# Kernel tuning notes

Hardware: AMD Instinct MI355X
Metric: run time of the kernel (lower is better)

Reference implementation:

```python
import jax, jax.numpy as jnp
import numpy as np

DIM = 128
KS = 7
HEADS = 4
HEAD_DIM = DIM // HEADS


def setup_inputs() -> dict:
    key = jax.random.key(0)
    ks = jax.random.split(key, 10)
    B, H, W, C = 4, 64, 64, DIM
    s = 0.02
    return {
        "x": jax.random.normal(ks[0], (B, H, W, C), jnp.float32),
        "qkv_w": jax.random.normal(ks[1], (C, 3 * C), jnp.float32) * s,
        "qkv_b": jnp.zeros((3 * C,), jnp.float32),
        "proj_w": jax.random.normal(ks[2], (C, C), jnp.float32) * s,
        "proj_b": jnp.zeros((C,), jnp.float32),
        "rpb": jax.random.normal(ks[3], (HEADS, 2 * KS - 1, 2 * KS - 1), jnp.float32) * s,
        "g1_w": jax.random.normal(ks[4], (C, C // 2), jnp.float32) * s,
        "g1_b": jnp.zeros((C // 2,), jnp.float32),
        "g2_w": jax.random.normal(ks[5], (C // 2, 1), jnp.float32) * s,
        "g2_b": jnp.zeros((1,), jnp.float32),
    }


def _neighborhood_attention(x, qkv_w, qkv_b, proj_w, proj_b, rpb):
    B, H, W, C = x.shape
    k = KS
    # qkv projection -> [B,H,W,3,heads,head_dim]
    qkv = (x @ qkv_w + qkv_b).reshape(B, H, W, 3, HEADS, HEAD_DIM)
    q = qkv[..., 0, :, :] * (HEAD_DIM ** -0.5)  # [B,H,W,h,d]
    kk = qkv[..., 1, :, :]
    v = qkv[..., 2, :, :]

    # Clamped sliding-window start indices (NATTEN semantics)
    sh = jnp.clip(jnp.arange(H) - k // 2, 0, H - k)  # [H]
    sw = jnp.clip(jnp.arange(W) - k // 2, 0, W - k)  # [W]
    idx_h = sh[:, None] + jnp.arange(k)[None, :]  # [H,k]
    idx_w = sw[:, None] + jnp.arange(k)[None, :]  # [W,k]

    # Gather neighborhood windows: [B,H,W,k,k,h,d]
    kwin = kk[:, idx_h[:, None, :, None], idx_w[None, :, None, :]]
    vwin = v[:, idx_h[:, None, :, None], idx_w[None, :, None, :]]

    # Relative position bias indices: (neighbor - query) + (k-1)
    bih = idx_h - jnp.arange(H)[:, None] + (k - 1)  # [H,k]
    biw = idx_w - jnp.arange(W)[:, None] + (k - 1)  # [W,k]
    # bias: [h,H,W,k,k] -> [H,W,h,k,k]
    bias = rpb[:, bih[:, None, :, None], biw[None, :, None, :]]
    bias = jnp.transpose(bias, (1, 2, 0, 3, 4))

    # scores: [B,H,W,h,k,k]
    scores = jnp.einsum('bxyhd,bxyklhd->bxyhkl', q, kwin) + bias[None]
    attn = jax.nn.softmax(scores.reshape(B, H, W, HEADS, k * k), axis=-1)
    attn = attn.reshape(B, H, W, HEADS, k, k)
    out = jnp.einsum('bxyhkl,bxyklhd->bxyhd', attn, vwin).reshape(B, H, W, C)
    return out @ proj_w + proj_b


def reference(x, qkv_w, qkv_b, proj_w, proj_b, rpb, g1_w, g1_b, g2_w, g2_b):
    attn_out = _neighborhood_attention(x, qkv_w, qkv_b, proj_w, proj_b, rpb)
    gate = jax.nn.sigmoid(jax.nn.relu(x @ g1_w + g1_b) @ g2_w + g2_b)  # [B,H,W,1]
    return attn_out * gate + x
```

## Files before the change

kernel.cpp:

```cpp
#include <hip/hip_runtime.h>
#include <hip/hip_bf16.h>
#include <math.h>

#define PIXELS 16384
#define C      128
#define KS     7
#define HEADS  4
#define HD     32
#define QSCALE 0.17677669529663687f

typedef __bf16 bf16x8 __attribute__((ext_vector_type(8)));
typedef float  f32x4  __attribute__((ext_vector_type(4)));

__device__ inline unsigned short f2bf(float f) {
    unsigned int u = __builtin_bit_cast(unsigned int, f);
    u += 0x7FFFu + ((u >> 16) & 1u);
    return (unsigned short)(u >> 16);
}
__device__ inline float bflo(unsigned int u) {
    return __builtin_bit_cast(float, u << 16);
}
__device__ inline float bfhi(unsigned int u) {
    return __builtin_bit_cast(float, u & 0xFFFF0000u);
}

__global__ __launch_bounds__(256) void prep_kernel(
    const float* __restrict__ x, const float* __restrict__ qkv_w,
    const float* __restrict__ g1_w, const float* __restrict__ qkv_b,
    const float* __restrict__ g1_b, const float* __restrict__ proj_w,
    unsigned short* __restrict__ xb, unsigned short* __restrict__ wT,
    unsigned short* __restrict__ pT, float* __restrict__ bias_ext)
{
    const int blk = blockIdx.x, tid = threadIdx.x;
    if (blk < 2048) {
        int base = blk * 1024 + tid * 4;
        float4 v = *(const float4*)(x + base);
        ushort4 o; o.x = f2bf(v.x); o.y = f2bf(v.y); o.z = f2bf(v.z); o.w = f2bf(v.w);
        *(ushort4*)(xb + base) = o;
    } else if (blk < 2104) {
        int n = (blk - 2048) * 8 + (tid >> 5);
        int kq = tid & 31;
        float f0, f1, f2, f3;
        if (n < 384) {
            f0 = qkv_w[(kq*4+0)*384 + n]; f1 = qkv_w[(kq*4+1)*384 + n];
            f2 = qkv_w[(kq*4+2)*384 + n]; f3 = qkv_w[(kq*4+3)*384 + n];
        } else {
            int nn = n - 384;
            f0 = g1_w[(kq*4+0)*64 + nn]; f1 = g1_w[(kq*4+1)*64 + nn];
            f2 = g1_w[(kq*4+2)*64 + nn]; f3 = g1_w[(kq*4+3)*64 + nn];
        }
        ushort4 o; o.x = f2bf(f0); o.y = f2bf(f1); o.z = f2bf(f2); o.w = f2bf(f3);
        *(ushort4*)(wT + n*128 + kq*4) = o;
    } else if (blk < 2120) {
        int n = (blk - 2104) * 8 + (tid >> 5);
        int kq = tid & 31;
        ushort4 o;
        o.x = f2bf(proj_w[(kq*4+0)*128 + n]);
        o.y = f2bf(proj_w[(kq*4+1)*128 + n]);
        o.z = f2bf(proj_w[(kq*4+2)*128 + n]);
        o.w = f2bf(proj_w[(kq*4+3)*128 + n]);
        *(ushort4*)(pT + n*128 + kq*4) = o;
    } else {
        for (int idx = tid; idx < 448; idx += 256)
            bias_ext[idx] = (idx < 384) ? qkv_b[idx] : g1_b[idx - 384];
    }
}

__global__ __launch_bounds__(256) void gemm_qkvh_fused(
    const unsigned short* __restrict__ xb, const unsigned short* __restrict__ wT,
    const float* __restrict__ bias_ext, const float* __restrict__ g2_w,
    const float* __restrict__ g2_b, unsigned short* __restrict__ qkvb,
    float* __restrict__ gate)
{
    __shared__ __align__(16) unsigned short As[64*128];
    __shared__ __align__(16) unsigned short Bs[64*128];
    const int nt = blockIdx.x;
    const int n0 = nt * 64;
    const int m0 = blockIdx.y * 64;
    const int tid = threadIdx.x;

#pragma unroll
    for (int it = 0; it < 4; it++) {
        int idx = tid + it*256, row = idx >> 4, c = idx & 15;
        uint4 v = *(const uint4*)(xb + (size_t)(m0+row)*128 + c*8);
        *(uint4*)(As + row*128 + ((c ^ (row&7)) << 3)) = v;
    }
#pragma unroll
    for (int it = 0; it < 4; it++) {
        int idx = tid + it*256, row = idx >> 4, c = idx & 15;
        uint4 v = *(const uint4*)(wT + (size_t)(n0+row)*128 + c*8);
        *(uint4*)(Bs + row*128 + ((c ^ (row&7)) << 3)) = v;
    }
    __syncthreads();

    const int wave = tid >> 6, lane = tid & 63;
    const int l15 = lane & 15, quad = lane >> 4;
    const int wm = (wave & 1) * 32, wn = (wave >> 1) * 32;

    f32x4 acc[2][2] = {};
#pragma unroll
    for (int ks = 0; ks < 4; ks++) {
        bf16x8 af[2], bq[2];
#pragma unroll
        for (int mt = 0; mt < 2; mt++) {
            int m = wm + mt*16 + l15;
            af[mt] = *(const bf16x8*)(As + m*128 + (((ks*4+quad) ^ (m&7)) << 3));
        }
#pragma unroll
        for (int ntl = 0; ntl < 2; ntl++) {
            int n = wn + ntl*16 + l15;
            bq[ntl] = *(const bf16x8*)(Bs + n*128 + (((ks*4+quad) ^ (n&7)) << 3));
        }
#pragma unroll
        for (int mt = 0; mt < 2; mt++)
#pragma unroll
            for (int ntl = 0; ntl < 2; ntl++)
                acc[mt][ntl] = __builtin_amdgcn_mfma_f32_16x16x32_bf16(
                    af[mt], bq[ntl], acc[mt][ntl], 0, 0, 0);
    }
    __syncthreads();

    if (nt < 6) {
        unsigned short* Cs = (unsigned short*)As;
#pragma unroll
        for (int ntl = 0; ntl < 2; ntl++) {
            int nl = wn + ntl*16 + l15;
            int ng = n0 + nl;
            float qs = (ng < 128) ? QSCALE : 1.0f;
            float bv = bias_ext[ng];
#pragma unroll
            for (int mt = 0; mt < 2; mt++)
#pragma unroll
                for (int r = 0; r < 4; r++) {
                    int ml = wm + mt*16 + quad*4 + r;
                    Cs[ml*64 + nl] = f2bf((acc[mt][ntl][r] + bv) * qs);
                }
        }
        __syncthreads();
        int row = tid >> 2, part = tid & 3;
        uint4 a = *(const uint4*)(Cs + row*64 + part*16);
        uint4 b = *(const uint4*)(Cs + row*64 + part*16 + 8);
        unsigned short* dst = qkvb + (size_t)(m0+row)*384 + n0 + part*16;
        *(uint4*)dst = a;
        *(uint4*)(dst + 8) = b;
    } else {
        float* gpart = (float*)Bs;
        float rs[2][4];
#pragma unroll
        for (int mt = 0; mt < 2; mt++)
#pragma unroll
            for (int r = 0; r < 4; r++) rs[mt][r] = 0.0f;
#pragma unroll
        for (int ntl = 0; ntl < 2; ntl++) {
            int nl = wn + ntl*16 + l15;
            float bv = bias_ext[384 + nl];
            float gw = g2_w[nl];
#pragma unroll
            for (int mt = 0; mt < 2; mt++)
#pragma unroll
                for (int r = 0; r < 4; r++) {
                    float h = acc[mt][ntl][r] + bv;
                    rs[mt][r] += fmaxf(h, 0.0f) * gw;
                }
        }
#pragma unroll
        for (int off = 1; off <= 8; off <<= 1)
#pragma unroll
            for (int mt = 0; mt < 2; mt++)
#pragma unroll
                for (int r = 0; r < 4; r++)
                    rs[mt][r] += __shfl_xor(rs[mt][r], off);
        if (l15 == 0) {
#pragma unroll
            for (int mt = 0; mt < 2; mt++)
#pragma unroll
                for (int r = 0; r < 4; r++)
                    gpart[(wave >> 1)*64 + wm + mt*16 + quad*4 + r] = rs[mt][r];
        }
        __syncthreads();
        if (tid < 64) {
            float g = gpart[tid] + gpart[64 + tid] + g2_b[0];
            gate[m0 + tid] = 1.0f / (1.0f + __expf(-g));
        }
    }
}

__global__ __launch_bounds__(256) void attn_kernel(
    const unsigned short* __restrict__ qkvb, const float* __restrict__ rpb,
    unsigned short* __restrict__ attnb)
{
    __shared__ __align__(16) unsigned short kvs[140 * 64];
    __shared__ float qf[32 * 32];
    __shared__ float rpb_lds[169];

    const int blk = blockIdx.x;
    const int h = blk & 3;
    const int tile = (blk >> 2) & 127;
    const int b = blk >> 9;
    const int tj0 = (tile & 15) * 4;
    const int ti0 = (tile >> 4) * 8;
    int wr0 = ti0 - 3; wr0 = wr0 < 0 ? 0 : (wr0 > 50 ? 50 : wr0);
    int wc0 = tj0 - 3; wc0 = wc0 < 0 ? 0 : (wc0 > 54 ? 54 : wc0);

    const int tid = threadIdx.x;

    if (tid < 169) rpb_lds[tid] = rpb[h * 169 + tid];

    if (tid < 128) {
        int pix = tid >> 2, jj = tid & 3;
        int pi = pix >> 2, pj = pix & 3;
        int gp = (b * 64 + ti0 + pi) * 64 + (tj0 + pj);
        uint4 u = *(const uint4*)(qkvb + (size_t)gp * 384 + h * 32 + jj * 8);
        float4 qa = { bflo(u.x), bfhi(u.x), bflo(u.y), bfhi(u.y) };
        float4 qb = { bflo(u.z), bfhi(u.z), bflo(u.w), bfhi(u.w) };
        *(float4*)(qf + pix*32 + jj*8)     = qa;
        *(float4*)(qf + pix*32 + jj*8 + 4) = qb;
    }
    for (int idx = tid; idx < 140 * 8; idx += 256) {
        int pos = idx >> 3, c = idx & 7;
        int rr = pos / 10, cc = pos - rr * 10;
        int gp = (b * 64 + wr0 + rr) * 64 + (wc0 + cc);
        int off = 128 + ((c >> 2) << 7) + h * 32 + ((c & 3) << 3);
        uint4 v = *(const uint4*)(qkvb + (size_t)gp * 384 + off);
        *(uint4*)(kvs + pos*64 + ((c ^ (pos & 7)) << 3)) = v;
    }
    __syncthreads();

    const int w = tid >> 6, lane = tid & 63;
    const int d4 = lane & 7, lg = lane >> 3;
    const int nr = (lane * 37) >> 8;
    const int nc = lane - nr * 7;

#pragma unroll 1
    for (int s = 0; s < 8; s++) {
        const int pix = w * 8 + s;
        const int pi = pix >> 2, pj = pix & 3;
        const int i = ti0 + pi, jx = tj0 + pj;
        int sh = i - 3; sh = sh < 0 ? 0 : (sh > 57 ? 57 : sh);
        int sw = jx - 3; sw = sw < 0 ? 0 : (sw > 57 ? 57 : sw);
        const int dr = sh - wr0, dc = sw - wc0;

        float e = 0.0f;
        if (lane < 49) {
            int pos = (dr + nr) * 10 + (dc + nc);
            int p7 = pos & 7;
            float acc = rpb_lds[(sh + nr - i + 6) * 13 + (sw + nc - jx + 6)];
            const float4* q4 = (const float4*)(qf + pix * 32);
#pragma unroll
            for (int c = 0; c < 4; c++) {
                uint4 k = *(const uint4*)(kvs + pos*64 + ((c ^ p7) << 3));
                float4 qa = q4[c*2], qb = q4[c*2+1];
                acc += qa.x*bflo(k.x) + qa.y*bfhi(k.x)
                     + qa.z*bflo(k.y) + qa.w*bfhi(k.y)
                     + qb.x*bflo(k.z) + qb.y*bfhi(k.z)
                     + qb.z*bflo(k.w) + qb.w*bfhi(k.w);
            }
            e = __expf(acc);
        }
        float sum = e;
#pragma unroll
        for (int off = 32; off >= 1; off >>= 1) sum += __shfl_xor(sum, off);
        const float a = e / sum;

        float4 acc4 = {0.f, 0.f, 0.f, 0.f};
#pragma unroll
        for (int t = 0; t < 7; t++) {
            int l = lg + 8 * t;
            float al = __shfl(a, l);
            int lr = (l * 37) >> 8, lc = l - lr * 7;
            int pos = (dr + lr) * 10 + (dc + lc);
            if (l >= 49) pos = 0;
            int p7 = pos & 7;
            uint2 v2 = *(const uint2*)(kvs + pos*64 +
                           (((4 + (d4 >> 1)) ^ p7) << 3) + ((d4 & 1) << 2));
            acc4.x += al * bflo(v2.x); acc4.y += al * bfhi(v2.x);
            acc4.z += al * bflo(v2.y); acc4.w += al * bfhi(v2.y);
        }
#pragma unroll
        for (int off = 8; off <= 32; off <<= 1) {
            acc4.x += __shfl_xor(acc4.x, off);
            acc4.y += __shfl_xor(acc4.y, off);
            acc4.z += __shfl_xor(acc4.z, off);
            acc4.w += __shfl_xor(acc4.w, off);
        }
        if (lg == 0) {
            int gp = (b * 64 + i) * 64 + jx;
            ushort4 o;
            o.x = f2bf(acc4.x); o.y = f2bf(acc4.y);
            o.z = f2bf(acc4.z); o.w = f2bf(acc4.w);
            *(ushort4*)(attnb + (size_t)gp * 128 + h * 32 + d4 * 4) = o;
        }
    }
}

__global__ __launch_bounds__(256) void gemm_proj_mfma(
    const unsigned short* __restrict__ ab, const unsigned short* __restrict__ pT,
    const float* __restrict__ proj_b, const float* __restrict__ gate,
    const float* __restrict__ x, float* __restrict__ out)
{
    __shared__ __align__(16) unsigned short As[64*128];
    __shared__ __align__(16) unsigned short Bs[64*128];
    const int n0 = blockIdx.x * 64;
    const int m0 = blockIdx.y * 64;
    const int tid = threadIdx.x;

#pragma unroll
    for (int it = 0; it < 4; it++) {
        int idx = tid + it*256, row = idx >> 4, c = idx & 15;
        uint4 v = *(const uint4*)(ab + (size_t)(m0+row)*128 + c*8);
        *(uint4*)(As + row*128 + ((c ^ (row&7)) << 3)) = v;
    }
#pragma unroll
    for (int it = 0; it < 4; it++) {
        int idx = tid + it*256, row = idx >> 4, c = idx & 15;
        uint4 v = *(const uint4*)(pT + (size_t)(n0+row)*128 + c*8);
        *(uint4*)(Bs + row*128 + ((c ^ (row&7)) << 3)) = v;
    }
    __syncthreads();

    const int wave = tid >> 6, lane = tid & 63;
    const int l15 = lane & 15, quad = lane >> 4;
    const int wm = (wave & 1) * 32, wn = (wave >> 1) * 32;

    f32x4 acc[2][2] = {};
#pragma unroll
    for (int ks = 0; ks < 4; ks++) {
        bf16x8 af[2], bq[2];
#pragma unroll
        for (int mt = 0; mt < 2; mt++) {
            int m = wm + mt*16 + l15;
            af[mt] = *(const bf16x8*)(As + m*128 + (((ks*4+quad) ^ (m&7)) << 3));
        }
#pragma unroll
        for (int ntl = 0; ntl < 2; ntl++) {
            int n = wn + ntl*16 + l15;
            bq[ntl] = *(const bf16x8*)(Bs + n*128 + (((ks*4+quad) ^ (n&7)) << 3));
        }
#pragma unroll
        for (int mt = 0; mt < 2; mt++)
#pragma unroll
            for (int ntl = 0; ntl < 2; ntl++)
                acc[mt][ntl] = __builtin_amdgcn_mfma_f32_16x16x32_bf16(
                    af[mt], bq[ntl], acc[mt][ntl], 0, 0, 0);
    }
    __syncthreads();

    float* Cs = (float*)As;
#pragma unroll
    for (int ntl = 0; ntl < 2; ntl++) {
        int nl = wn + ntl*16 + l15;
        float bv = proj_b[n0 + nl];
#pragma unroll
        for (int mt = 0; mt < 2; mt++)
#pragma unroll
            for (int r = 0; r < 4; r++) {
                int ml = wm + mt*16 + quad*4 + r;
                Cs[ml*64 + nl] = acc[mt][ntl][r] + bv;
            }
    }
    __syncthreads();
    int row = tid >> 2, part = tid & 3;
    float gv = gate[m0 + row];
    const float* xr = x + (size_t)(m0+row)*128 + n0 + part*16;
    float* orow = out + (size_t)(m0+row)*128 + n0 + part*16;
#pragma unroll
    for (int q = 0; q < 4; q++) {
        float4 cv = *(const float4*)(Cs + row*64 + part*16 + q*4);
        float4 xv = *(const float4*)(xr + q*4);
        float4 o;
        o.x = cv.x * gv + xv.x; o.y = cv.y * gv + xv.y;
        o.z = cv.z * gv + xv.z; o.w = cv.w * gv + xv.w;
        *(float4*)(orow + q*4) = o;
    }
}

extern "C" void kernel_launch(void* const* d_in, const int* in_sizes, int n_in,
                              void* d_out, int out_size, void* d_ws, size_t ws_size,
                              hipStream_t stream)
{
    const float* x      = (const float*)d_in[0];
    const float* qkv_w  = (const float*)d_in[1];
    const float* qkv_b  = (const float*)d_in[2];
    const float* proj_w = (const float*)d_in[3];
    const float* proj_b = (const float*)d_in[4];
    const float* rpb    = (const float*)d_in[5];
    const float* g1_w   = (const float*)d_in[6];
    const float* g1_b   = (const float*)d_in[7];
    const float* g2_w   = (const float*)d_in[8];
    const float* g2_b   = (const float*)d_in[9];
    float* out = (float*)d_out;

    float* ws        = (float*)d_ws;
    float* gate      = ws;
    float* bias_ext  = gate + 16384;
    unsigned short* xb    = (unsigned short*)(bias_ext + 448);
    unsigned short* wT    = xb + 2097152;
    unsigned short* pT    = wT + 57344;
    unsigned short* qkvb  = pT + 16384;
    unsigned short* attnb = qkvb + 6291456;

    (void)in_sizes; (void)n_in; (void)out_size; (void)ws_size;

    prep_kernel<<<2121, 256, 0, stream>>>(x, qkv_w, g1_w, qkv_b, g1_b, proj_w,
                                          xb, wT, pT, bias_ext);
    gemm_qkvh_fused<<<dim3(7, 256), 256, 0, stream>>>(xb, wT, bias_ext,
                                                      g2_w, g2_b, qkvb, gate);
    attn_kernel<<<2048, 256, 0, stream>>>(qkvb, rpb, attnb);
    gemm_proj_mfma<<<dim3(2, 256), 256, 0, stream>>>(attnb, pT, proj_b, gate, x, out);
}
```

Measured before the change: 134.9 us.

## Restructure neighborhood attention to one thread per query pixel

The attention kernel now gives each thread a whole query pixel. The thread keeps q and a 32-wide output accumulator in registers and loops over all 49 neighbours, running an online softmax sum with no max subtraction. This replaces the old lane-per-neighbour layout with its cross-lane shuffle reductions. Blocks now cover 8x8 pixel tiles for two heads, with a 14x14 K/V halo in LDS, and the launch changes to 512 blocks of 128 threads. This cuts shuffles and reduces redundant halo loads, at the cost of higher register pressure, fewer blocks (low occupancy on a large GPU), and unswizzled LDS reads that may hit bank conflicts.

After: 125.1 us. 7.3% less time.

```diff
diff --git a/kernel.cpp b/kernel.cpp
--- a/kernel.cpp
+++ b/kernel.cpp
@@ -185,112 +185,114 @@
     }
 }
 
-__global__ __launch_bounds__(256) void attn_kernel(
+__global__ __launch_bounds__(128) void attn_kernel(
     const unsigned short* __restrict__ qkvb, const float* __restrict__ rpb,
     unsigned short* __restrict__ attnb)
 {
-    __shared__ __align__(16) unsigned short kvs[140 * 64];
-    __shared__ float qf[32 * 32];
-    __shared__ float rpb_lds[169];
+    __shared__ __align__(16) unsigned short kvs[196 * 136];
+    __shared__ float rpb_lds[2 * 169];
 
     const int blk = blockIdx.x;
-    const int h = blk & 3;
-    const int tile = (blk >> 2) & 127;
-    const int b = blk >> 9;
-    const int tj0 = (tile & 15) * 4;
-    const int ti0 = (tile >> 4) * 8;
-    int wr0 = ti0 - 3; wr0 = wr0 < 0 ? 0 : (wr0 > 50 ? 50 : wr0);
-    int wc0 = tj0 - 3; wc0 = wc0 < 0 ? 0 : (wc0 > 54 ? 54 : wc0);
+    const int pr = blk & 1;
+    const int tile = (blk >> 1) & 63;
+    const int b = blk >> 7;
+    const int ti0 = (tile >> 3) * 8, tj0 = (tile & 7) * 8;
+    int wr0 = ti0 - 3; if (wr0 < 0) wr0 = 0;
+    int wc0 = tj0 - 3; if (wc0 < 0) wc0 = 0;
 
     const int tid = threadIdx.x;
 
-    if (tid < 169) rpb_lds[tid] = rpb[h * 169 + tid];
-
-    if (tid < 128) {
-        int pix = tid >> 2, jj = tid & 3;
-        int pi = pix >> 2, pj = pix & 3;
-        int gp = (b * 64 + ti0 + pi) * 64 + (tj0 + pj);
-        uint4 u = *(const uint4*)(qkvb + (size_t)gp * 384 + h * 32 + jj * 8);
-        float4 qa = { bflo(u.x), bfhi(u.x), bflo(u.y), bfhi(u.y) };
-        float4 qb = { bflo(u.z), bfhi(u.z), bflo(u.w), bfhi(u.w) };
-        *(float4*)(qf + pix*32 + jj*8)     = qa;
-        *(float4*)(qf + pix*32 + jj*8 + 4) = qb;
-    }
-    for (int idx = tid; idx < 140 * 8; idx += 256) {
-        int pos = idx >> 3, c = idx & 7;
-        int rr = pos / 10, cc = pos - rr * 10;
-        int gp = (b * 64 + wr0 + rr) * 64 + (wc0 + cc);
-        int off = 128 + ((c >> 2) << 7) + h * 32 + ((c & 3) << 3);
-        uint4 v = *(const uint4*)(qkvb + (size_t)gp * 384 + off);
-        *(uint4*)(kvs + pos*64 + ((c ^ (pos & 7)) << 3)) = v;
-    }
-    __syncthreads();
-
-    const int w = tid >> 6, lane = tid & 63;
-    const int d4 = lane & 7, lg = lane >> 3;
-    const int nr = (lane * 37) >> 8;
-    const int nc = lane - nr * 7;
-
-#pragma unroll 1
-    for (int s = 0; s < 8; s++) {
-        const int pix = w * 8 + s;
-        const int pi = pix >> 2, pj = pix & 3;
-        const int i = ti0 + pi, jx = tj0 + pj;
-        int sh = i - 3; sh = sh < 0 ? 0 : (sh > 57 ? 57 : sh);
-        int sw = jx - 3; sw = sw < 0 ? 0 : (sw > 57 ? 57 : sw);
-        const int dr = sh - wr0, dc = sw - wc0;
-
-        float e = 0.0f;
-        if (lane < 49) {
-            int pos = (dr + nr) * 10 + (dc + nc);
-            int p7 = pos & 7;
-            float acc = rpb_lds[(sh + nr - i + 6) * 13 + (sw + nc - jx + 6)];
-            const float4* q4 = (const float4*)(qf + pix * 32);
-#pragma unroll
-            for (int c = 0; c < 4; c++) {
-                uint4 k = *(const uint4*)(kvs + pos*64 + ((c ^ p7) << 3));
-                float4 qa = q4[c*2], qb = q4[c*2+1];
-                acc += qa.x*bflo(k.x) + qa.y*bfhi(k.x)
-                     + qa.z*bflo(k.y) + qa.w*bfhi(k.y)
-                     + qb.x*bflo(k.z) + qb.y*bfhi(k.z)
-                     + qb.z*bflo(k.w) + qb.w*bfhi(k.w);
+    for (int t = tid; t < 338; t += 128) rpb_lds[t] = rpb[pr * 338 + t];
+
+    for (int idx = tid; idx < 196 * 16; idx += 128) {
+        int pos = idx >> 4, t = idx & 15;
+        int wr = pos / 14, wc = pos - wr * 14;
+        int gr = wr0 + wr; if (gr > 63) gr = 63;
+        int gc = wc0 + wc; if (gc > 63) gc = 63;
+        size_t gp = (size_t)(((b << 6) + gr) << 6) + gc;
+        int src = 128 + ((t >> 3) << 7) + pr * 64 + ((t & 7) << 3);
+        uint4 v = *(const uint4*)(qkvb + gp * 384 + src);
+        *(uint4*)(kvs + pos * 136 + ((t >> 3) << 6) + ((t & 7) << 3)) = v;
+    }
+    __syncthreads();
+
+    const int hh = tid >> 6, lane = tid & 63;
+    const int h = pr * 2 + hh;
+    const int pi = lane >> 3, pj = lane & 7;
+    const int i = ti0 + pi, j = tj0 + pj;
+    int sh = i - 3; sh = sh < 0 ? 0 : (sh > 57 ? 57 : sh);
+    int sw = j - 3; sw = sw < 0 ? 0 : (sw > 57 ? 57 : sw);
+    const int dr = sh - wr0, dc = sw - wc0;
+    const size_t gp = (size_t)(((b << 6) + i) << 6) + j;
+
+    unsigned int qu[16];
+    const unsigned short* qptr = qkvb + gp * 384 + h * 32;
+    *(uint4*)(qu + 0)  = *(const uint4*)(qptr + 0);
+    *(uint4*)(qu + 4)  = *(const uint4*)(qptr + 8);
+    *(uint4*)(qu + 8)  = *(const uint4*)(qptr + 16);
+    *(uint4*)(qu + 12) = *(const uint4*)(qptr + 24);
+    float qf[32];
+#pragma unroll
+    for (int p = 0; p < 16; p++) {
+        qf[2*p]   = bflo(qu[p]);
+        qf[2*p+1] = bfhi(qu[p]);
+    }
+
+    float acc[32];
+#pragma unroll
+    for (int d = 0; d < 32; d++) acc[d] = 0.0f;
+    float ssum = 0.0f;
+
+    const float* rl = rpb_lds + hh * 169;
+    const int rbase = (sh - i + 6) * 13 + (sw - j + 6);
+    const int hwbase = (dr * 14 + dc) * 136 + hh * 32;
+
+    for (int kr = 0; kr < 7; kr++) {
+        int hw = hwbase + kr * (14 * 136);
+        int ri = rbase + kr * 13;
+#pragma unroll
+        for (int kc = 0; kc < 7; kc++) {
+            const unsigned short* kp = kvs + hw;
+            unsigned int ku[16];
+            *(uint4*)(ku + 0)  = *(const uint4*)(kp + 0);
+            *(uint4*)(ku + 4)  = *(const uint4*)(kp + 8);
+            *(uint4*)(ku + 8)  = *(const uint4*)(kp + 16);
+            *(uint4*)(ku + 12) = *(const uint4*)(kp + 24);
+            float s0 = rl[ri + kc], s1 = 0.0f;
+#pragma unroll
+            for (int p = 0; p < 8; p++) {
+                s0 += qf[2*p]      * bflo(ku[p])     + qf[2*p+1]  * bfhi(ku[p]);
+                s1 += qf[2*p+16]   * bflo(ku[p+8])   + qf[2*p+17] * bfhi(ku[p+8]);
             }
-            e = __expf(acc);
-        }
-        float sum = e;
-#pragma unroll
-        for (int off = 32; off >= 1; off >>= 1) sum += __shfl_xor(sum, off);
-        const float a = e / sum;
-
-        float4 acc4 = {0.f, 0.f, 0.f, 0.f};
-#pragma unroll
-        for (int t = 0; t < 7; t++) {
-            int l = lg + 8 * t;
-            float al = __shfl(a, l);
-            int lr = (l * 37) >> 8, lc = l - lr * 7;
-            int pos = (dr + lr) * 10 + (dc + lc);
-            if (l >= 49) pos = 0;
-            int p7 = pos & 7;
-            uint2 v2 = *(const uint2*)(kvs + pos*64 +
-                           (((4 + (d4 >> 1)) ^ p7) << 3) + ((d4 & 1) << 2));
-            acc4.x += al * bflo(v2.x); acc4.y += al * bfhi(v2.x);
-            acc4.z += al * bflo(v2.y); acc4.w += al * bfhi(v2.y);
-        }
-#pragma unroll
-        for (int off = 8; off <= 32; off <<= 1) {
-            acc4.x += __shfl_xor(acc4.x, off);
-            acc4.y += __shfl_xor(acc4.y, off);
-            acc4.z += __shfl_xor(acc4.z, off);
-            acc4.w += __shfl_xor(acc4.w, off);
-        }
-        if (lg == 0) {
-            int gp = (b * 64 + i) * 64 + jx;
-            ushort4 o;
-            o.x = f2bf(acc4.x); o.y = f2bf(acc4.y);
-            o.z = f2bf(acc4.z); o.w = f2bf(acc4.w);
-            *(ushort4*)(attnb + (size_t)gp * 128 + h * 32 + d4 * 4) = o;
-        }
-    }
+            float e = __expf(s0 + s1);
+            ssum += e;
+            unsigned int vu[16];
+            *(uint4*)(vu + 0)  = *(const uint4*)(kp + 64);
+            *(uint4*)(vu + 4)  = *(const uint4*)(kp + 72);
+            *(uint4*)(vu + 8)  = *(const uint4*)(kp + 80);
+            *(uint4*)(vu + 12) = *(const uint4*)(kp + 88);
+#pragma unroll
+            for (int p = 0; p < 16; p++) {
+                acc[2*p]   += e * bflo(vu[p]);
+                acc[2*p+1] += e * bfhi(vu[p]);
+            }
+            hw += 136;
+        }
+    }
+
+    const float inv = 1.0f / ssum;
+    unsigned int o[16];
+#pragma unroll
+    for (int p = 0; p < 16; p++) {
+        unsigned int lo = f2bf(acc[2*p] * inv);
+        unsigned int hi = f2bf(acc[2*p+1] * inv);
+        o[p] = lo | (hi << 16);
+    }
+    unsigned short* op = attnb + gp * 128 + h * 32;
+    *(uint4*)(op + 0)  = *(const uint4*)(o + 0);
+    *(uint4*)(op + 8)  = *(const uint4*)(o + 4);
+    *(uint4*)(op + 16) = *(const uint4*)(o + 8);
+    *(uint4*)(op + 24) = *(const uint4*)(o + 12);
 }
 
 __global__ __launch_bounds__(256) void gemm_proj_mfma(
@@ -405,6 +407,6 @@
                                           xb, wT, pT, bias_ext);
     gemm_qkvh_fused<<<dim3(7, 256), 256, 0, stream>>>(xb, wT, bias_ext,
                                                       g2_w, g2_b, qkvb, gate);
-    attn_kernel<<<2048, 256, 0, stream>>>(qkvb, rpb, attnb);
+    attn_kernel<<<512, 128, 0, stream>>>(qkvb, rpb, attnb);
     gemm_proj_mfma<<<dim3(2, 256), 256, 0, stream>>>(attnb, pT, proj_b, gate, x, out);
 }
```
